# Performance work log

Measured on AMD Instinct MI355X. Metric: run time of the kernel, lower is better.

## Reference

```python
import jax, jax.numpy as jnp
import numpy as np

N_NODES = 100000
N_EDGES = 1600000
D_IN = 128
D_HID = 128
D_OUT = 40


def _linear_init(key, fan_in, fan_out):
    # torch nn.Linear default: U(-1/sqrt(fan_in), 1/sqrt(fan_in)) for W and b
    kw, kb = jax.random.split(key)
    bound = 1.0 / np.sqrt(fan_in)
    W = jax.random.uniform(kw, (fan_in, fan_out), jnp.float32, -bound, bound)
    b = jax.random.uniform(kb, (fan_out,), jnp.float32, -bound, bound)
    return W, b


def setup_inputs() -> dict:
    key = jax.random.key(0)
    ks = jax.random.split(key, 8)
    x = jax.random.normal(ks[0], (N_NODES, D_IN), jnp.float32)
    edges = jax.random.randint(ks[1], (2, N_EDGES), 0, N_NODES, jnp.int64)
    # layer 0: MLP(128 -> 128 -> 128)
    W1_0, b1_0 = _linear_init(ks[2], D_IN, D_HID)
    W2_0, b2_0 = _linear_init(ks[3], D_HID, D_HID)
    # layer 1: MLP(128 -> 128 -> 128)
    W1_1, b1_1 = _linear_init(ks[4], D_HID, D_HID)
    W2_1, b2_1 = _linear_init(ks[5], D_HID, D_HID)
    # layer 2: MLP(128 -> 128 -> 40)
    W1_2, b1_2 = _linear_init(ks[6], D_HID, D_HID)
    W2_2, b2_2 = _linear_init(ks[7], D_HID, D_OUT)
    eps = jnp.zeros(())  # GINConv train_eps=True initializes eps=0
    return {
        "x": x, "edges": edges,
        "W1_0": W1_0, "b1_0": b1_0, "W2_0": W2_0, "b2_0": b2_0, "eps_0": eps,
        "W1_1": W1_1, "b1_1": b1_1, "W2_1": W2_1, "b2_1": b2_1, "eps_1": eps,
        "W1_2": W1_2, "b1_2": b1_2, "W2_2": W2_2, "b2_2": b2_2, "eps_2": eps,
    }


def _gin_conv(x, src, dst, eps, W1, b1, W2, b2):
    # sum-aggregate neighbor features: out_i = MLP((1+eps)*x_i + sum_{j->i} x_j)
    aggr = jax.ops.segment_sum(x[src], dst, num_segments=x.shape[0])
    h = (1.0 + eps) * x + aggr
    h = jnp.maximum(h @ W1 + b1, 0.0)  # MLP layer 1 + ReLU
    return h @ W2 + b2                  # MLP layer 2


def reference(x, edges,
              W1_0, b1_0, W2_0, b2_0, eps_0,
              W1_1, b1_1, W2_1, b2_1, eps_1,
              W1_2, b1_2, W2_2, b2_2, eps_2):
    src, dst = edges[0], edges[1]
    # dropout is identity at inference (training=False)
    h = jax.nn.relu(_gin_conv(x, src, dst, eps_0, W1_0, b1_0, W2_0, b2_0))
    h = jax.nn.relu(_gin_conv(h, src, dst, eps_1, W1_1, b1_1, W2_1, b2_1))
    o = _gin_conv(h, src, dst, eps_2, W1_2, b1_2, W2_2, b2_2)
    return jax.nn.log_softmax(o, axis=1)
```

## Files before the change

### kernel.cpp

```cpp
#include <hip/hip_runtime.h>
#include <stdint.h>

typedef __attribute__((ext_vector_type(8))) short short8;
typedef __attribute__((ext_vector_type(4))) short short4v;
typedef __attribute__((ext_vector_type(4))) float float4v;

__device__ __forceinline__ float bf2f(unsigned short s) {
    union { unsigned int u; float f; } c; c.u = ((unsigned int)s) << 16; return c.f;
}
__device__ __forceinline__ unsigned short f2bf(float f) {
    union { float f; unsigned int u; } c; c.f = f;
    unsigned int x = c.u;
    unsigned int r = x + 0x7fffu + ((x >> 16) & 1u);
    return (unsigned short)(r >> 16);
}
__device__ __forceinline__ void unpack2(unsigned int u, float& lo, float& hi) {
    union { unsigned int uu; float ff; } a, b;
    a.uu = u << 16;
    b.uu = u & 0xffff0000u;
    lo = a.ff; hi = b.ff;
}

__global__ __launch_bounds__(256) void bs_count(const int* __restrict__ dst, int nE,
                                                int* __restrict__ bucketCnt) {
    __shared__ int c[512];
    int t = threadIdx.x;
    for (int i = t; i < 512; i += 256) c[i] = 0;
    __syncthreads();
    int base = blockIdx.x * 4096;
    for (int i = t; i < 4096; i += 256) {
        int e = base + i;
        if (e < nE) atomicAdd(&c[dst[e] >> 8], 1);
    }
    __syncthreads();
    for (int i = t; i < 512; i += 256)
        if (c[i]) atomicAdd(&bucketCnt[i], c[i]);
}

__global__ __launch_bounds__(512) void bs_scan(const int* __restrict__ bucketCnt,
                                               int* __restrict__ bucketBase,
                                               int* __restrict__ bucketCur,
                                               int* __restrict__ off, int M, int nE) {
    __shared__ int s[512];
    int t = threadIdx.x;
    int v = bucketCnt[t];
    s[t] = v;
    __syncthreads();
    for (int o = 1; o < 512; o <<= 1) {
        int x = (t >= o) ? s[t - o] : 0;
        __syncthreads();
        s[t] += x;
        __syncthreads();
    }
    bucketBase[t] = s[t] - v;
    bucketCur[t] = s[t] - v;
    if (t == 511) bucketBase[512] = s[511];
    if (t == 0) off[M] = nE;
}

__global__ __launch_bounds__(512) void bs_scatter(const int* __restrict__ src,
                                                  const int* __restrict__ dst, int nE,
                                                  int* __restrict__ bucketCur,
                                                  unsigned int* __restrict__ ebuf) {
    __shared__ int cnt[512];
    __shared__ int excl[512];
    __shared__ int chunk[512];
    __shared__ unsigned int buf[4096];
    __shared__ unsigned short bkt[4096];
    int t = threadIdx.x;
    cnt[t] = 0;
    __syncthreads();
    int base = blockIdx.x * 4096;
    int n = nE - base; if (n > 4096) n = 4096;
    unsigned int pk[8]; int bk[8]; int rk[8];
#pragma unroll
    for (int u = 0; u < 8; ++u) {
        int i = t + u * 512;
        if (i < n) {
            int e = base + i;
            int d = dst[e];
            int b = d >> 8;
            bk[u] = b;
            pk[u] = (unsigned int)src[e] | ((unsigned int)(d & 255) << 17);
            rk[u] = atomicAdd(&cnt[b], 1);
        } else bk[u] = -1;
    }
    __syncthreads();
    excl[t] = cnt[t];
    __syncthreads();
    for (int o = 1; o < 512; o <<= 1) {
        int x = (t >= o) ? excl[t - o] : 0;
        __syncthreads();
        excl[t] += x;
        __syncthreads();
    }
    int ex = excl[t] - cnt[t];
    __syncthreads();
    excl[t] = ex;
    if (cnt[t]) chunk[t] = atomicAdd(&bucketCur[t], cnt[t]);
    __syncthreads();
#pragma unroll
    for (int u = 0; u < 8; ++u) {
        if (bk[u] >= 0) {
            int lp = excl[bk[u]] + rk[u];
            buf[lp] = pk[u];
            bkt[lp] = (unsigned short)bk[u];
        }
    }
    __syncthreads();
    for (int i = t; i < n; i += 512) {
        int b = bkt[i];
        ebuf[chunk[b] + (i - excl[b])] = buf[i];
    }
}

__global__ __launch_bounds__(512) void bs_build(const unsigned int* __restrict__ ebuf,
                                                const int* __restrict__ bucketBase,
                                                int* __restrict__ off,
                                                int* __restrict__ esrc, int M) {
    __shared__ int cnt[256];
    __shared__ int excl[256];
    __shared__ int obuf[5120];
    int t = threadIdx.x, b = blockIdx.x;
    int base = bucketBase[b];
    int n = bucketBase[b + 1] - base;
    if (t < 256) cnt[t] = 0;
    __syncthreads();
    unsigned int pk[10]; int dl[10]; int rk[10];
#pragma unroll
    for (int u = 0; u < 10; ++u) {
        int i = t + u * 512;
        if (i < n) {
            unsigned int p = ebuf[base + i];
            pk[u] = p;
            int d = (p >> 17) & 255;
            dl[u] = d;
            rk[u] = atomicAdd(&cnt[d], 1);
        } else dl[u] = -1;
    }
    __syncthreads();
    if (t < 256) excl[t] = cnt[t];
    __syncthreads();
    for (int o = 1; o < 256; o <<= 1) {
        int x = (t < 256 && t >= o) ? excl[t - o] : 0;
        __syncthreads();
        if (t < 256) excl[t] += x;
        __syncthreads();
    }
    if (t < 256) {
        int ex = excl[t] - cnt[t];
        int node = b * 256 + t;
        if (node < M) off[node] = base + ex;
        excl[t] = ex;
    }
    __syncthreads();
#pragma unroll
    for (int u = 0; u < 10; ++u) {
        if (dl[u] >= 0) {
            int lp = excl[dl[u]] + rk[u];
            if (lp < 5120) obuf[lp] = (int)(pk[u] & 0x1FFFF);
        }
    }
    __syncthreads();
    for (int i = t; i < n; i += 512) esrc[base + i] = obuf[i];
}

struct Prep {
    const float* W[6];
    unsigned short* hi[6];
    const float4* xin;
    uint2* xout;
    int n4;
    int* bucketCnt;
};

__global__ __launch_bounds__(256) void k_prep(Prep p) {
    int b = blockIdx.x;
    if (b == 0) {
        p.bucketCnt[threadIdx.x] = 0;
        p.bucketCnt[threadIdx.x + 256] = 0;
    }
    if (b < 344) {
        int mat = b >> 6;
        int rel = b - mat * 64;
        int NPAD = (mat == 5) ? 48 : 128;
        int N = (mat == 5) ? 40 : 128;
        int idx = rel * 256 + threadIdx.x;
        if (idx >= NPAD * 128) return;
        int n = idx >> 7, k = idx & 127;
        float w = (n < N) ? p.W[mat][k * N + n] : 0.f;
        p.hi[mat][idx] = f2bf(w);
    } else {
        int i = (b - 344) * 256 + threadIdx.x;
        if (i >= p.n4) return;
        float4 v = p.xin[i];
        uint2 o;
        o.x = ((unsigned int)f2bf(v.y) << 16) | f2bf(v.x);
        o.y = ((unsigned int)f2bf(v.w) << 16) | f2bf(v.z);
        p.xout[i] = o;
    }
}

__device__ __forceinline__ void acc8(uint4 v, float* s) {
    float a, b;
    unpack2(v.x, a, b); s[0] += a; s[1] += b;
    unpack2(v.y, a, b); s[2] += a; s[3] += b;
    unpack2(v.z, a, b); s[4] += a; s[5] += b;
    unpack2(v.w, a, b); s[6] += a; s[7] += b;
}

__global__ __launch_bounds__(256) void k_aggr(const uint4* __restrict__ Hin,
                                              const int* __restrict__ off,
                                              const int* __restrict__ esrc,
                                              const float* __restrict__ epsp,
                                              uint4* __restrict__ Ahi, int M) {
    int w = threadIdx.x >> 6, lane = threadIdx.x & 63;
    int li = lane & 15, q = lane >> 4;
    int node = blockIdx.x * 16 + w * 4 + q;
    if (node >= M) return;
    float ep = 1.0f + epsp[0];
    uint4 ow = Hin[node * 16 + li];
    float s[8] = {0.f, 0.f, 0.f, 0.f, 0.f, 0.f, 0.f, 0.f};
    int i = off[node], e = off[node + 1];
    int idx[8];
    if (i + 8 <= e) {
#pragma unroll
        for (int j = 0; j < 8; ++j) idx[j] = esrc[i + j];
    }
    while (i + 8 <= e) {
        uint4 v[8];
#pragma unroll
        for (int j = 0; j < 8; ++j) v[j] = Hin[idx[j] * 16 + li];
        int inext = i + 8;
        if (inext + 8 <= e) {
#pragma unroll
            for (int j = 0; j < 8; ++j) idx[j] = esrc[inext + j];
        }
#pragma unroll
        for (int j = 0; j < 8; ++j) acc8(v[j], s);
        i = inext;
    }
    if (i < e) {
        int last = e - 1;
        uint4 v[8];
#pragma unroll
        for (int j = 0; j < 8; ++j) {
            int k = i + j;
            int cl = k < last ? k : last;
            v[j] = Hin[esrc[cl] * 16 + li];
        }
#pragma unroll
        for (int j = 0; j < 8; ++j) {
            bool ok = (i + j) < e;
            uint4 u;
            u.x = ok ? v[j].x : 0u;
            u.y = ok ? v[j].y : 0u;
            u.z = ok ? v[j].z : 0u;
            u.w = ok ? v[j].w : 0u;
            acc8(u, s);
        }
    }
    float o[8];
    unpack2(ow.x, o[0], o[1]);
    unpack2(ow.y, o[2], o[3]);
    unpack2(ow.z, o[4], o[5]);
    unpack2(ow.w, o[6], o[7]);
#pragma unroll
    for (int k = 0; k < 8; ++k) s[k] = ep * o[k] + s[k];
    uint4 r;
    r.x = ((unsigned int)f2bf(s[1]) << 16) | f2bf(s[0]);
    r.y = ((unsigned int)f2bf(s[3]) << 16) | f2bf(s[2]);
    r.z = ((unsigned int)f2bf(s[5]) << 16) | f2bf(s[4]);
    r.w = ((unsigned int)f2bf(s[7]) << 16) | f2bf(s[6]);
    Ahi[node * 16 + li] = r;
}

template <int NT2, bool LOGITS>
__global__ __launch_bounds__(256, 2) void k_mlp(const unsigned short* __restrict__ AhiS,
                                                const unsigned short* __restrict__ W1h,
                                                const float* __restrict__ B1,
                                                const unsigned short* __restrict__ W2h,
                                                const float* __restrict__ B2,
                                                unsigned short* __restrict__ HOut,
                                                float* __restrict__ LOut, int M) {
    __shared__ short wbuf[128 * 136];
    int t = threadIdx.x, w = t >> 6, lane = t & 63;
    int lm = lane & 15, lg = lane >> 4;
    int rbase = blockIdx.x * 128;

    short8 xf2[2][4];
    bool act[2];
#pragma unroll
    for (int t2 = 0; t2 < 2; ++t2) {
        int r0 = rbase + t2 * 64 + w * 16;
        act[t2] = (r0 < M);
        if (act[t2]) {
            const short* Xp = (const short*)AhiS + (r0 + lm) * 128 + lg * 8;
#pragma unroll
            for (int kb = 0; kb < 4; ++kb) xf2[t2][kb] = *(const short8*)(Xp + kb * 32);
        } else {
#pragma unroll
            for (int kb = 0; kb < 4; ++kb) xf2[t2][kb] = (short8){0,0,0,0,0,0,0,0};
        }
    }
    constexpr int W2CH = (NT2 * 16 * 128) / 2048;
    short8 w1r[8], w2r[W2CH];
#pragma unroll
    for (int u = 0; u < 8; ++u) w1r[u] = *(const short8*)(W1h + t * 8 + u * 2048);
#pragma unroll
    for (int u = 0; u < W2CH; ++u) w2r[u] = *(const short8*)(W2h + t * 8 + u * 2048);

#pragma unroll
    for (int u = 0; u < 8; ++u) {
        int i = t * 8 + u * 2048;
        *(short8*)&wbuf[(i >> 7) * 136 + (i & 127)] = w1r[u];
    }
    __syncthreads();

    short4v h2[2][8];
#pragma unroll
    for (int t2 = 0; t2 < 2; ++t2) {
        float4v acc1[8];
#pragma unroll
        for (int nt = 0; nt < 8; ++nt) acc1[nt] = (float4v){0.f, 0.f, 0.f, 0.f};
#pragma unroll
        for (int nt = 0; nt < 8; ++nt) {
#pragma unroll
            for (int kb = 0; kb < 4; ++kb) {
                short8 wf = *(const short8*)&wbuf[(nt * 16 + lm) * 136 + kb * 32 + lg * 8];
                acc1[nt] = __builtin_amdgcn_mfma_f32_16x16x32_bf16(wf, xf2[t2][kb], acc1[nt], 0, 0, 0);
            }
        }
#pragma unroll
        for (int nt = 0; nt < 8; ++nt) {
            float4 b1 = *(const float4*)(B1 + nt * 16 + lg * 4);
            float v0 = acc1[nt][0] + b1.x; v0 = v0 > 0.f ? v0 : 0.f;
            float v1 = acc1[nt][1] + b1.y; v1 = v1 > 0.f ? v1 : 0.f;
            float v2 = acc1[nt][2] + b1.z; v2 = v2 > 0.f ? v2 : 0.f;
            float v3 = acc1[nt][3] + b1.w; v3 = v3 > 0.f ? v3 : 0.f;
            h2[t2][nt] = (short4v){(short)f2bf(v0), (short)f2bf(v1),
                                   (short)f2bf(v2), (short)f2bf(v3)};
        }
    }

    __syncthreads();
#pragma unroll
    for (int u = 0; u < W2CH; ++u) {
        int i = t * 8 + u * 2048;
        *(short8*)&wbuf[(i >> 7) * 136 + (i & 127)] = w2r[u];
    }
    __syncthreads();

    float4v acc2[2][NT2];
#pragma unroll
    for (int t2 = 0; t2 < 2; ++t2)
#pragma unroll
        for (int ot = 0; ot < NT2; ++ot) acc2[t2][ot] = (float4v){0.f, 0.f, 0.f, 0.f};
#pragma unroll
    for (int ot = 0; ot < NT2; ++ot) {
#pragma unroll
        for (int nt = 0; nt < 8; ++nt) {
            short4v wf = *(const short4v*)&wbuf[(ot * 16 + lm) * 136 + nt * 16 + lg * 4];
#pragma unroll
            for (int t2 = 0; t2 < 2; ++t2)
                acc2[t2][ot] = __builtin_amdgcn_mfma_f32_16x16x16bf16_1k(wf, h2[t2][nt],
                                                                         acc2[t2][ot], 0, 0, 0);
        }
    }

#pragma unroll
    for (int t2 = 0; t2 < 2; ++t2) {
        if (!act[t2]) continue;
        int row = rbase + t2 * 64 + w * 16 + lm;
        if (!LOGITS) {
#pragma unroll
            for (int ot = 0; ot < NT2; ++ot) {
                float4 b2 = *(const float4*)(B2 + ot * 16 + lg * 4);
                float v0 = acc2[t2][ot][0] + b2.x; v0 = v0 > 0.f ? v0 : 0.f;
                float v1 = acc2[t2][ot][1] + b2.y; v1 = v1 > 0.f ? v1 : 0.f;
                float v2 = acc2[t2][ot][2] + b2.z; v2 = v2 > 0.f ? v2 : 0.f;
                float v3 = acc2[t2][ot][3] + b2.w; v3 = v3 > 0.f ? v3 : 0.f;
                uint2 pk;
                pk.x = ((unsigned int)f2bf(v1) << 16) | f2bf(v0);
                pk.y = ((unsigned int)f2bf(v3) << 16) | f2bf(v2);
                *(uint2*)(HOut + row * 128 + ot * 16 + lg * 4) = pk;
            }
        } else {
            float vv[NT2][4];
#pragma unroll
            for (int ot = 0; ot < NT2; ++ot) {
                int ub = ot * 16 + lg * 4;
                bool valid = ub <= 36;
                float4 b2 = valid ? *(const float4*)(B2 + ub) : (float4){0.f, 0.f, 0.f, 0.f};
                vv[ot][0] = valid ? acc2[t2][ot][0] + b2.x : -1e30f;
                vv[ot][1] = valid ? acc2[t2][ot][1] + b2.y : -1e30f;
                vv[ot][2] = valid ? acc2[t2][ot][2] + b2.z : -1e30f;
                vv[ot][3] = valid ? acc2[t2][ot][3] + b2.w : -1e30f;
            }
            float m = -1e30f;
#pragma unroll
            for (int ot = 0; ot < NT2; ++ot)
#pragma unroll
                for (int r = 0; r < 4; ++r) m = fmaxf(m, vv[ot][r]);
            m = fmaxf(m, __shfl_xor(m, 16, 64));
            m = fmaxf(m, __shfl_xor(m, 32, 64));
            float s = 0.f;
#pragma unroll
            for (int ot = 0; ot < NT2; ++ot)
#pragma unroll
                for (int r = 0; r < 4; ++r)
                    s += (vv[ot][r] > -1e29f) ? expf(vv[ot][r] - m) : 0.f;
            s += __shfl_xor(s, 16, 64);
            s += __shfl_xor(s, 32, 64);
            float ls = m + logf(s);
#pragma unroll
            for (int ot = 0; ot < NT2; ++ot) {
                int ub = ot * 16 + lg * 4;
                if (ub <= 36) {
                    float4 outv = {vv[ot][0] - ls, vv[ot][1] - ls,
                                   vv[ot][2] - ls, vv[ot][3] - ls};
                    *(float4*)(LOut + row * 40 + ub) = outv;
                }
            }
        }
    }
}

extern "C" void kernel_launch(void* const* d_in, const int* in_sizes, int n_in,
                              void* d_out, int out_size, void* d_ws, size_t ws_size,
                              hipStream_t stream) {
    const float* x    = (const float*)d_in[0];
    const int*   edges = (const int*)d_in[1];
    const float* eps0 = (const float*)d_in[6];
    const float* eps1 = (const float*)d_in[11];
    const float* eps2 = (const float*)d_in[16];
    const float* B1[3] = {(const float*)d_in[3], (const float*)d_in[8], (const float*)d_in[13]};
    const float* B2[3] = {(const float*)d_in[5], (const float*)d_in[10], (const float*)d_in[15]};

    int M  = in_sizes[0] / 128;
    int nE = in_sizes[1] / 2;
    const int* e_src = edges;
    const int* e_dst = edges + nE;

    char* ws = (char*)d_ws;
    size_t o = 0;
    auto alloc = [&](size_t bytes) {
        size_t p = o;
        o = (o + bytes + 511) & ~(size_t)511;
        return ws + p;
    };
    int* bucketCnt  = (int*)alloc(512 * 4);
    int* bucketBase = (int*)alloc(513 * 4);
    int* bucketCur  = (int*)alloc(512 * 4);
    int* off  = (int*)alloc((size_t)(M + 1) * 4);
    int* esrc = (int*)alloc((size_t)nE * 4);
    unsigned int* ebuf = (unsigned int*)alloc((size_t)nE * 4);

    Prep pp;
    pp.W[0] = (const float*)d_in[2];  pp.W[1] = (const float*)d_in[4];
    pp.W[2] = (const float*)d_in[7];  pp.W[3] = (const float*)d_in[9];
    pp.W[4] = (const float*)d_in[12]; pp.W[5] = (const float*)d_in[14];
    for (int m = 0; m < 6; ++m) {
        int npad = (m == 5) ? 48 : 128;
        pp.hi[m] = (unsigned short*)alloc((size_t)npad * 128 * 2);
    }
    unsigned short* xb  = (unsigned short*)alloc((size_t)M * 128 * 2);
    unsigned short* Ahi = (unsigned short*)alloc((size_t)M * 128 * 2);
    unsigned short* Hb  = (unsigned short*)alloc((size_t)M * 128 * 2);
    pp.xin = (const float4*)x;
    pp.xout = (uint2*)xb;
    pp.n4 = M * 32;
    pp.bucketCnt = bucketCnt;
    (void)ws_size; (void)n_in; (void)out_size;

    int nChunk = (nE + 4095) / 4096;
    int nBk = (M + 255) / 256;
    k_prep<<<344 + (pp.n4 + 255) / 256, 256, 0, stream>>>(pp);
    bs_count<<<nChunk, 256, 0, stream>>>(e_dst, nE, bucketCnt);
    bs_scan<<<1, 512, 0, stream>>>(bucketCnt, bucketBase, bucketCur, off, M, nE);
    bs_scatter<<<nChunk, 512, 0, stream>>>(e_src, e_dst, nE, bucketCur, ebuf);
    bs_build<<<nBk, 512, 0, stream>>>(ebuf, bucketBase, off, esrc, M);

    int gA = (M + 15) / 16;
    int gG = (M + 127) / 128;

    k_aggr<<<gA, 256, 0, stream>>>((const uint4*)xb, off, esrc, eps0, (uint4*)Ahi, M);
    k_mlp<8, false><<<gG, 256, 0, stream>>>(Ahi, pp.hi[0], B1[0],
                                            pp.hi[1], B2[0], Hb, nullptr, M);
    k_aggr<<<gA, 256, 0, stream>>>((const uint4*)Hb, off, esrc, eps1, (uint4*)Ahi, M);
    k_mlp<8, false><<<gG, 256, 0, stream>>>(Ahi, pp.hi[2], B1[1],
                                            pp.hi[3], B2[1], Hb, nullptr, M);
    k_aggr<<<gA, 256, 0, stream>>>((const uint4*)Hb, off, esrc, eps2, (uint4*)Ahi, M);
    k_mlp<3, true><<<gG, 256, 0, stream>>>(Ahi, pp.hi[4], B1[2],
                                           pp.hi[5], B2[2], nullptr,
                                           (float*)d_out, M);
}
```

Before: 405.3 us.

## Fuse neighbor aggregation into the MLP kernel via shared-memory staging

Result: no change. 412.7 us (+1.8%).

```diff
diff --git a/kernel.cpp b/kernel.cpp
--- a/kernel.cpp
+++ b/kernel.cpp
@@ -209,112 +209,115 @@
     unpack2(v.w, a, b); s[6] += a; s[7] += b;
 }
 
-__global__ __launch_bounds__(256) void k_aggr(const uint4* __restrict__ Hin,
-                                              const int* __restrict__ off,
-                                              const int* __restrict__ esrc,
-                                              const float* __restrict__ epsp,
-                                              uint4* __restrict__ Ahi, int M) {
-    int w = threadIdx.x >> 6, lane = threadIdx.x & 63;
-    int li = lane & 15, q = lane >> 4;
-    int node = blockIdx.x * 16 + w * 4 + q;
-    if (node >= M) return;
-    float ep = 1.0f + epsp[0];
-    uint4 ow = Hin[node * 16 + li];
-    float s[8] = {0.f, 0.f, 0.f, 0.f, 0.f, 0.f, 0.f, 0.f};
-    int i = off[node], e = off[node + 1];
-    int idx[8];
-    if (i + 8 <= e) {
-#pragma unroll
-        for (int j = 0; j < 8; ++j) idx[j] = esrc[i + j];
-    }
-    while (i + 8 <= e) {
-        uint4 v[8];
-#pragma unroll
-        for (int j = 0; j < 8; ++j) v[j] = Hin[idx[j] * 16 + li];
-        int inext = i + 8;
-        if (inext + 8 <= e) {
-#pragma unroll
-            for (int j = 0; j < 8; ++j) idx[j] = esrc[inext + j];
-        }
-#pragma unroll
-        for (int j = 0; j < 8; ++j) acc8(v[j], s);
-        i = inext;
-    }
-    if (i < e) {
-        int last = e - 1;
-        uint4 v[8];
-#pragma unroll
-        for (int j = 0; j < 8; ++j) {
-            int k = i + j;
-            int cl = k < last ? k : last;
-            v[j] = Hin[esrc[cl] * 16 + li];
-        }
-#pragma unroll
-        for (int j = 0; j < 8; ++j) {
-            bool ok = (i + j) < e;
-            uint4 u;
-            u.x = ok ? v[j].x : 0u;
-            u.y = ok ? v[j].y : 0u;
-            u.z = ok ? v[j].z : 0u;
-            u.w = ok ? v[j].w : 0u;
-            acc8(u, s);
-        }
-    }
-    float o[8];
-    unpack2(ow.x, o[0], o[1]);
-    unpack2(ow.y, o[2], o[3]);
-    unpack2(ow.z, o[4], o[5]);
-    unpack2(ow.w, o[6], o[7]);
-#pragma unroll
-    for (int k = 0; k < 8; ++k) s[k] = ep * o[k] + s[k];
-    uint4 r;
-    r.x = ((unsigned int)f2bf(s[1]) << 16) | f2bf(s[0]);
-    r.y = ((unsigned int)f2bf(s[3]) << 16) | f2bf(s[2]);
-    r.z = ((unsigned int)f2bf(s[5]) << 16) | f2bf(s[4]);
-    r.w = ((unsigned int)f2bf(s[7]) << 16) | f2bf(s[6]);
-    Ahi[node * 16 + li] = r;
-}
-
 template <int NT2, bool LOGITS>
-__global__ __launch_bounds__(256, 2) void k_mlp(const unsigned short* __restrict__ AhiS,
-                                                const unsigned short* __restrict__ W1h,
-                                                const float* __restrict__ B1,
-                                                const unsigned short* __restrict__ W2h,
-                                                const float* __restrict__ B2,
-                                                unsigned short* __restrict__ HOut,
-                                                float* __restrict__ LOut, int M) {
-    __shared__ short wbuf[128 * 136];
+__global__ __launch_bounds__(256, 2) void k_fused(const uint4* __restrict__ Hin,
+                                                  const int* __restrict__ off,
+                                                  const int* __restrict__ esrc,
+                                                  const float* __restrict__ epsp,
+                                                  const unsigned short* __restrict__ W1h,
+                                                  const float* __restrict__ B1,
+                                                  const unsigned short* __restrict__ W2h,
+                                                  const float* __restrict__ B2,
+                                                  unsigned short* __restrict__ HOut,
+                                                  float* __restrict__ LOut, int M) {
+    __shared__ short sbuf[128 * 136];
     int t = threadIdx.x, w = t >> 6, lane = t & 63;
     int lm = lane & 15, lg = lane >> 4;
     int rbase = blockIdx.x * 128;
+    float ep = 1.0f + epsp[0];
+
+    short8 w1r[8];
+#pragma unroll
+    for (int u = 0; u < 8; ++u) w1r[u] = *(const short8*)(W1h + t * 8 + u * 2048);
+
+    bool act[2];
+    act[0] = (rbase + w * 16) < M;
+    act[1] = (rbase + 64 + w * 16) < M;
+
+#pragma unroll
+    for (int t2 = 0; t2 < 2; ++t2) {
+        for (int rr = 0; rr < 4; ++rr) {
+            int row = t2 * 64 + w * 16 + rr * 4 + lg;
+            uint4 r;
+            if (act[t2]) {
+                int node = rbase + row;
+                float s[8] = {0.f, 0.f, 0.f, 0.f, 0.f, 0.f, 0.f, 0.f};
+                int i = off[node], e = off[node + 1];
+                int idx[8];
+                if (i + 8 <= e) {
+#pragma unroll
+                    for (int j = 0; j < 8; ++j) idx[j] = esrc[i + j];
+                }
+                while (i + 8 <= e) {
+                    uint4 v[8];
+#pragma unroll
+                    for (int j = 0; j < 8; ++j) v[j] = Hin[idx[j] * 16 + lm];
+                    int inext = i + 8;
+                    if (inext + 8 <= e) {
+#pragma unroll
+                        for (int j = 0; j < 8; ++j) idx[j] = esrc[inext + j];
+                    }
+#pragma unroll
+                    for (int j = 0; j < 8; ++j) acc8(v[j], s);
+                    i = inext;
+                }
+                if (i < e) {
+                    int last = e - 1;
+                    uint4 v[8];
+#pragma unroll
+                    for (int j = 0; j < 8; ++j) {
+                        int k = i + j;
+                        int cl = k < last ? k : last;
+                        v[j] = Hin[esrc[cl] * 16 + lm];
+                    }
+#pragma unroll
+                    for (int j = 0; j < 8; ++j) {
+                        bool ok = (i + j) < e;
+                        uint4 u2;
+                        u2.x = ok ? v[j].x : 0u;
+                        u2.y = ok ? v[j].y : 0u;
+                        u2.z = ok ? v[j].z : 0u;
+                        u2.w = ok ? v[j].w : 0u;
+                        acc8(u2, s);
+                    }
+                }
+                uint4 ow = Hin[node * 16 + lm];
+                float o[8];
+                unpack2(ow.x, o[0], o[1]);
+                unpack2(ow.y, o[2], o[3]);
+                unpack2(ow.z, o[4], o[5]);
+                unpack2(ow.w, o[6], o[7]);
+#pragma unroll
+                for (int k = 0; k < 8; ++k) s[k] = ep * o[k] + s[k];
+                r.x = ((unsigned int)f2bf(s[1]) << 16) | f2bf(s[0]);
+                r.y = ((unsigned int)f2bf(s[3]) << 16) | f2bf(s[2]);
+                r.z = ((unsigned int)f2bf(s[5]) << 16) | f2bf(s[4]);
+                r.w = ((unsigned int)f2bf(s[7]) << 16) | f2bf(s[6]);
+            } else {
+                r.x = 0u; r.y = 0u; r.z = 0u; r.w = 0u;
+            }
+            *(uint4*)&sbuf[row * 136 + lm * 8] = r;
+        }
+    }
+    __syncthreads();
 
     short8 xf2[2][4];
-    bool act[2];
-#pragma unroll
-    for (int t2 = 0; t2 < 2; ++t2) {
-        int r0 = rbase + t2 * 64 + w * 16;
-        act[t2] = (r0 < M);
-        if (act[t2]) {
-            const short* Xp = (const short*)AhiS + (r0 + lm) * 128 + lg * 8;
-#pragma unroll
-            for (int kb = 0; kb < 4; ++kb) xf2[t2][kb] = *(const short8*)(Xp + kb * 32);
-        } else {
-#pragma unroll
-            for (int kb = 0; kb < 4; ++kb) xf2[t2][kb] = (short8){0,0,0,0,0,0,0,0};
-        }
-    }
-    constexpr int W2CH = (NT2 * 16 * 128) / 2048;
-    short8 w1r[8], w2r[W2CH];
-#pragma unroll
-    for (int u = 0; u < 8; ++u) w1r[u] = *(const short8*)(W1h + t * 8 + u * 2048);
-#pragma unroll
-    for (int u = 0; u < W2CH; ++u) w2r[u] = *(const short8*)(W2h + t * 8 + u * 2048);
+#pragma unroll
+    for (int t2 = 0; t2 < 2; ++t2)
+#pragma unroll
+        for (int kb = 0; kb < 4; ++kb)
+            xf2[t2][kb] = *(const short8*)&sbuf[(t2 * 64 + w * 16 + lm) * 136 + kb * 32 + lg * 8];
+    __syncthreads();
 
 #pragma unroll
     for (int u = 0; u < 8; ++u) {
         int i = t * 8 + u * 2048;
-        *(short8*)&wbuf[(i >> 7) * 136 + (i & 127)] = w1r[u];
-    }
+        *(short8*)&sbuf[(i >> 7) * 136 + (i & 127)] = w1r[u];
+    }
+    constexpr int W2CH = (NT2 * 16 * 128) / 2048;
+    short8 w2r[W2CH];
+#pragma unroll
+    for (int u = 0; u < W2CH; ++u) w2r[u] = *(const short8*)(W2h + t * 8 + u * 2048);
     __syncthreads();
 
     short4v h2[2][8];
@@ -327,7 +330,7 @@
         for (int nt = 0; nt < 8; ++nt) {
 #pragma unroll
             for (int kb = 0; kb < 4; ++kb) {
-                short8 wf = *(const short8*)&wbuf[(nt * 16 + lm) * 136 + kb * 32 + lg * 8];
+                short8 wf = *(const short8*)&sbuf[(nt * 16 + lm) * 136 + kb * 32 + lg * 8];
                 acc1[nt] = __builtin_amdgcn_mfma_f32_16x16x32_bf16(wf, xf2[t2][kb], acc1[nt], 0, 0, 0);
             }
         }
@@ -347,7 +350,7 @@
 #pragma unroll
     for (int u = 0; u < W2CH; ++u) {
         int i = t * 8 + u * 2048;
-        *(short8*)&wbuf[(i >> 7) * 136 + (i & 127)] = w2r[u];
+        *(short8*)&sbuf[(i >> 7) * 136 + (i & 127)] = w2r[u];
     }
     __syncthreads();
 
@@ -360,7 +363,7 @@
     for (int ot = 0; ot < NT2; ++ot) {
 #pragma unroll
         for (int nt = 0; nt < 8; ++nt) {
-            short4v wf = *(const short4v*)&wbuf[(ot * 16 + lm) * 136 + nt * 16 + lg * 4];
+            short4v wf = *(const short4v*)&sbuf[(ot * 16 + lm) * 136 + nt * 16 + lg * 4];
 #pragma unroll
             for (int t2 = 0; t2 < 2; ++t2)
                 acc2[t2][ot] = __builtin_amdgcn_mfma_f32_16x16x16bf16_1k(wf, h2[t2][nt],
@@ -465,8 +468,8 @@
         pp.hi[m] = (unsigned short*)alloc((size_t)npad * 128 * 2);
     }
     unsigned short* xb  = (unsigned short*)alloc((size_t)M * 128 * 2);
-    unsigned short* Ahi = (unsigned short*)alloc((size_t)M * 128 * 2);
     unsigned short* Hb  = (unsigned short*)alloc((size_t)M * 128 * 2);
+    unsigned short* Hb2 = (unsigned short*)alloc((size_t)M * 128 * 2);
     pp.xin = (const float4*)x;
     pp.xout = (uint2*)xb;
     pp.n4 = M * 32;
@@ -481,17 +484,15 @@
     bs_scatter<<<nChunk, 512, 0, stream>>>(e_src, e_dst, nE, bucketCur, ebuf);
     bs_build<<<nBk, 512, 0, stream>>>(ebuf, bucketBase, off, esrc, M);
 
-    int gA = (M + 15) / 16;
     int gG = (M + 127) / 128;
 
-    k_aggr<<<gA, 256, 0, stream>>>((const uint4*)xb, off, esrc, eps0, (uint4*)Ahi, M);
-    k_mlp<8, false><<<gG, 256, 0, stream>>>(Ahi, pp.hi[0], B1[0],
-                                            pp.hi[1], B2[0], Hb, nullptr, M);
-    k_aggr<<<gA, 256, 0, stream>>>((const uint4*)Hb, off, esrc, eps1, (uint4*)Ahi, M);
-    k_mlp<8, false><<<gG, 256, 0, stream>>>(Ahi, pp.hi[2], B1[1],
-                                            pp.hi[3], B2[1], Hb, nullptr, M);
-    k_aggr<<<gA, 256, 0, stream>>>((const uint4*)Hb, off, esrc, eps2, (uint4*)Ahi, M);
-    k_mlp<3, true><<<gG, 256, 0, stream>>>(Ahi, pp.hi[4], B1[2],
-                                           pp.hi[5], B2[2], nullptr,
-                                           (float*)d_out, M);
-}
+    k_fused<8, false><<<gG, 256, 0, stream>>>((const uint4*)xb, off, esrc, eps0,
+                                              pp.hi[0], B1[0], pp.hi[1], B2[0],
+                                              Hb, nullptr, M);
+    k_fused<8, false><<<gG, 256, 0, stream>>>((const uint4*)Hb, off, esrc, eps1,
+                                              pp.hi[2], B1[1], pp.hi[3], B2[1],
+                                              Hb2, nullptr, M);
+    k_fused<3, true><<<gG, 256, 0, stream>>>((const uint4*)Hb2, off, esrc, eps2,
+                                             pp.hi[4], B1[2], pp.hi[5], B2[2],
+                                             nullptr, (float*)d_out, M);
+}
```
